# Optimization experiments

Hardware: AMD Instinct MI355X
Metric: run time of the kernel (lower is better)

Reference implementation:

```python
import jax, jax.numpy as jnp
import numpy as np

B, T, DIM = 2, 1024, 4096
H, Hk, D = 32, 8, 128
NREP = H // Hk
SCALE = 1.0 / np.sqrt(D)
LAMBDA_INIT = 0.8 - 0.6 * np.exp(-0.3 * 0)  # layer_idx=0 -> 0.2
EPS = 1e-6


def setup_inputs() -> dict:
    key = jax.random.key(0)
    ks = jax.random.split(key, 12)
    x = jax.random.normal(ks[0], (B, T, DIM), dtype=jnp.float32)
    cos = jax.random.uniform(ks[1], (T, D // 2), dtype=jnp.float32)
    sin = jax.random.uniform(ks[2], (T, D // 2), dtype=jnp.float32)
    wq = jax.random.normal(ks[3], (DIM, 2 * H * D), dtype=jnp.float32) * 0.02
    wk = jax.random.normal(ks[4], (DIM, 2 * Hk * D), dtype=jnp.float32) * 0.02
    wv = jax.random.normal(ks[5], (DIM, Hk * D), dtype=jnp.float32) * 0.02
    wo = jax.random.normal(ks[6], (H * D, DIM), dtype=jnp.float32) * 0.02
    lambda_q1 = jax.random.normal(ks[7], (H, D), dtype=jnp.float32) * 0.1
    lambda_k1 = jax.random.normal(ks[8], (H, D), dtype=jnp.float32) * 0.1
    lambda_q2 = jax.random.normal(ks[9], (H, D), dtype=jnp.float32) * 0.1
    lambda_k2 = jax.random.normal(ks[10], (H, D), dtype=jnp.float32) * 0.1
    subln_w = jnp.ones((D,), dtype=jnp.float32)
    return {"x": x, "cos": cos, "sin": sin, "wq": wq, "wk": wk, "wv": wv,
            "wo": wo, "lambda_q1": lambda_q1, "lambda_k1": lambda_k1,
            "lambda_q2": lambda_q2, "lambda_k2": lambda_k2, "subln_w": subln_w}


def _rope(xh, cos, sin):
    # xh: [B, h, T, D]; cos/sin: [T, D/2]
    x1, x2 = xh[..., : D // 2], xh[..., D // 2:]
    c = cos[None, None, :, :]
    s = sin[None, None, :, :]
    return jnp.concatenate([x1 * c - x2 * s, x2 * c + x1 * s], axis=-1)


def _causal_attn(q, k, v):
    # q,k,v: [B, H, T, D]
    s = jnp.einsum("bhqd,bhkd->bhqk", q, k) * SCALE
    causal = jnp.tril(jnp.ones((T, T), dtype=bool))
    s = jnp.where(causal[None, None], s, jnp.finfo(s.dtype).min)
    p = jax.nn.softmax(s, axis=-1)
    return jnp.einsum("bhqk,bhkd->bhqd", p, v)


def reference(x, cos, sin, wq, wk, wv, wo, lambda_q1, lambda_k1, lambda_q2, lambda_k2, subln_w):
    q_full = (x @ wq).reshape(B, T, 2 * H, D).transpose(0, 2, 1, 3)   # [B,2H,T,D]
    k_full = (x @ wk).reshape(B, T, 2 * Hk, D).transpose(0, 2, 1, 3)  # [B,2Hk,T,D]
    v = (x @ wv).reshape(B, T, Hk, D).transpose(0, 2, 1, 3)           # [B,Hk,T,D]

    q1, q2 = q_full[:, :H], q_full[:, H:]
    k1, k2 = k_full[:, :Hk], k_full[:, Hk:]

    q1 = _rope(q1, cos, sin)
    q2 = _rope(q2, cos, sin)
    k1 = _rope(k1, cos, sin)
    k2 = _rope(k2, cos, sin)

    def expand_kv(kv):  # [B,Hk,T,D] -> [B,H,T,D] (GQA repeat)
        return jnp.repeat(kv, NREP, axis=1)

    k1e, k2e, ve = expand_kv(k1), expand_kv(k2), expand_kv(v)

    a1 = _causal_attn(q1, k1e, ve)
    a2 = _causal_attn(q2, k2e, ve)

    lam = (jnp.exp(jnp.sum(lambda_q1 * lambda_k1, axis=-1))
           - jnp.exp(jnp.sum(lambda_q2 * lambda_k2, axis=-1))
           + LAMBDA_INIT)  # [H]
    diff = a1 - lam[None, :, None, None] * a2  # [B,H,T,D]

    # per-head-dim RMSNorm (subln)
    rms = jax.lax.rsqrt(jnp.mean(diff * diff, axis=-1, keepdims=True) + EPS)
    diff = diff * rms * subln_w

    out = diff.transpose(0, 2, 1, 3).reshape(B, T, H * D)
    return out @ wo
```

## Files before the change

### kernel.cpp

```cpp
#include <hip/hip_runtime.h>
#include <hip/hip_bf16.h>
#include <stdint.h>

typedef unsigned short u16;
typedef unsigned int u32;
typedef short bf16x8 __attribute__((ext_vector_type(8)));
typedef float f32x4 __attribute__((ext_vector_type(4)));

#define SCALE_F 0.088388347648318447f
#define LAMBDA_INIT_F 0.2f

__device__ __forceinline__ u16 f2bf(float f) {
  union { float f; u32 u; } v; v.f = f;
  u32 r = v.u + 0x7fffu + ((v.u >> 16) & 1u);
  return (u16)(r >> 16);
}
__device__ __forceinline__ float bf2f(u16 u) {
  union { u32 u; float f; } v; v.u = ((u32)u) << 16;
  return v.f;
}

typedef __attribute__((address_space(1))) void gvoid_t;
typedef __attribute__((address_space(3))) void lvoid_t;
__device__ __forceinline__ void gload16(const void* g, void* l) {
  __builtin_amdgcn_global_load_lds((gvoid_t*)g, (lvoid_t*)l, 16, 0, 0);
}

__global__ void cast_f32_bf16(const float4* __restrict__ in, uint2* __restrict__ out, int n4) {
  int i = blockIdx.x * 256 + threadIdx.x;
  if (i >= n4) return;
  float4 v = in[i];
  uint2 o;
  o.x = (u32)f2bf(v.x) | ((u32)f2bf(v.y) << 16);
  o.y = (u32)f2bf(v.z) | ((u32)f2bf(v.w) << 16);
  out[i] = o;
}

__global__ void trans_cast(const float* __restrict__ in, u16* __restrict__ out, int K, int N) {
  __shared__ float tile[32][33];
  int kt = blockIdx.y * 32, nt = blockIdx.x * 32;
  int x = threadIdx.x, y = threadIdx.y;
  #pragma unroll
  for (int j = 0; j < 32; j += 8)
    tile[y + j][x] = in[(size_t)(kt + y + j) * N + nt + x];
  __syncthreads();
  #pragma unroll
  for (int j = 0; j < 32; j += 8)
    out[(size_t)(nt + y + j) * K + kt + x] = f2bf(tile[x][y + j]);
}

#define STA(buf, t) { \
  gload16(Ab + (size_t)(t) * 64, (buf) + dsloc); \
  gload16(Ab + (size_t)32 * K + (size_t)(t) * 64, (buf) + 2048 + dsloc); \
  gload16(Ab + (size_t)64 * K + (size_t)(t) * 64, (buf) + 4096 + dsloc); \
  gload16(Ab + (size_t)96 * K + (size_t)(t) * 64, (buf) + 6144 + dsloc); }
#define STB(buf, t) { \
  gload16(Bb + (size_t)(t) * 64, (buf) + dsloc); \
  gload16(Bb + (size_t)32 * K + (size_t)(t) * 64, (buf) + 2048 + dsloc); \
  gload16(Bb + (size_t)64 * K + (size_t)(t) * 64, (buf) + 4096 + dsloc); \
  gload16(Bb + (size_t)96 * K + (size_t)(t) * 64, (buf) + 6144 + dsloc); }
#define MFMA16 { \
  acc[0][0] = __builtin_amdgcn_mfma_f32_16x16x32_bf16(a0, b0, acc[0][0], 0, 0, 0); \
  acc[0][1] = __builtin_amdgcn_mfma_f32_16x16x32_bf16(a0, b1, acc[0][1], 0, 0, 0); \
  acc[0][2] = __builtin_amdgcn_mfma_f32_16x16x32_bf16(a0, b2, acc[0][2], 0, 0, 0); \
  acc[0][3] = __builtin_amdgcn_mfma_f32_16x16x32_bf16(a0, b3, acc[0][3], 0, 0, 0); \
  acc[1][0] = __builtin_amdgcn_mfma_f32_16x16x32_bf16(a1, b0, acc[1][0], 0, 0, 0); \
  acc[1][1] = __builtin_amdgcn_mfma_f32_16x16x32_bf16(a1, b1, acc[1][1], 0, 0, 0); \
  acc[1][2] = __builtin_amdgcn_mfma_f32_16x16x32_bf16(a1, b2, acc[1][2], 0, 0, 0); \
  acc[1][3] = __builtin_amdgcn_mfma_f32_16x16x32_bf16(a1, b3, acc[1][3], 0, 0, 0); \
  acc[2][0] = __builtin_amdgcn_mfma_f32_16x16x32_bf16(a2, b0, acc[2][0], 0, 0, 0); \
  acc[2][1] = __builtin_amdgcn_mfma_f32_16x16x32_bf16(a2, b1, acc[2][1], 0, 0, 0); \
  acc[2][2] = __builtin_amdgcn_mfma_f32_16x16x32_bf16(a2, b2, acc[2][2], 0, 0, 0); \
  acc[2][3] = __builtin_amdgcn_mfma_f32_16x16x32_bf16(a2, b3, acc[2][3], 0, 0, 0); \
  acc[3][0] = __builtin_amdgcn_mfma_f32_16x16x32_bf16(a3, b0, acc[3][0], 0, 0, 0); \
  acc[3][1] = __builtin_amdgcn_mfma_f32_16x16x32_bf16(a3, b1, acc[3][1], 0, 0, 0); \
  acc[3][2] = __builtin_amdgcn_mfma_f32_16x16x32_bf16(a3, b2, acc[3][2], 0, 0, 0); \
  acc[3][3] = __builtin_amdgcn_mfma_f32_16x16x32_bf16(a3, b3, acc[3][3], 0, 0, 0); }

template <bool OUT_BF16>
__global__ __launch_bounds__(256, 2) void gemm8p(const u16* __restrict__ A,
                                                 const u16* __restrict__ Bt,
                                                 void* __restrict__ Cv,
                                                 int M, int N, int K, int TN) {
  extern __shared__ u16 lds[];
  const int tid = threadIdx.x;
  const int lane = tid & 63;
  const int wid = tid >> 6;
  const int wm = wid >> 1, wn = wid & 1;
  const int ln = lane & 15, gr = lane >> 4;
  const int NT = K >> 6;

  const int bid = blockIdx.x;
  const int bn = (bid % TN) * 128;
  const int bm = (bid / TN) * 128;

  const int srow = tid >> 3;
  const int sch = (tid & 7) ^ (srow & 7);
  const u16* Ab = A + (size_t)(bm + srow) * K + sch * 8;
  const u16* Bb = Bt + (size_t)(bn + srow) * K + sch * 8;
  const int dsloc = tid * 8;

  const int aro = (wm * 64 + ln) * 64;
  const int bro = (wn * 64 + ln) * 64;
  const int c0 = (gr ^ (ln & 7)) * 8;
  const int c1 = ((4 + gr) ^ (ln & 7)) * 8;

  f32x4 acc[4][4] = {};
  bf16x8 a0, a1, a2, a3, b0, b1, b2, b3;

  STA(lds, 0);
  STB(lds + 16384, 0);
  STB(lds + 24576, 1);
  asm volatile("s_waitcnt vmcnt(4)" ::: "memory");
  __builtin_amdgcn_s_barrier();

  int tm3 = 0;
  for (int t = 0; t < NT; ++t) {
    const u16* Ac = lds + (t & 1) * 8192;
    u16* An = lds + ((t + 1) & 1) * 8192;
    const u16* Bc = lds + 16384 + tm3 * 8192;
    int tn3 = tm3 + 2; if (tn3 >= 3) tn3 -= 3;
    u16* Bn = lds + 16384 + tn3 * 8192;

    a0 = *(const bf16x8*)&Ac[aro + c0];
    a1 = *(const bf16x8*)&Ac[aro + 1024 + c0];
    a2 = *(const bf16x8*)&Ac[aro + 2048 + c0];
    a3 = *(const bf16x8*)&Ac[aro + 3072 + c0];
    b0 = *(const bf16x8*)&Bc[bro + c0];
    b1 = *(const bf16x8*)&Bc[bro + 1024 + c0];
    b2 = *(const bf16x8*)&Bc[bro + 2048 + c0];
    b3 = *(const bf16x8*)&Bc[bro + 3072 + c0];
    if (t + 1 < NT) STA(An, t + 1);
    __builtin_amdgcn_s_barrier();
    __builtin_amdgcn_s_setprio(1);
    MFMA16;
    __builtin_amdgcn_s_setprio(0);
    __builtin_amdgcn_s_barrier();

    a0 = *(const bf16x8*)&Ac[aro + c1];
    a1 = *(const bf16x8*)&Ac[aro + 1024 + c1];
    a2 = *(const bf16x8*)&Ac[aro + 2048 + c1];
    a3 = *(const bf16x8*)&Ac[aro + 3072 + c1];
    b0 = *(const bf16x8*)&Bc[bro + c1];
    b1 = *(const bf16x8*)&Bc[bro + 1024 + c1];
    b2 = *(const bf16x8*)&Bc[bro + 2048 + c1];
    b3 = *(const bf16x8*)&Bc[bro + 3072 + c1];
    if (t + 2 < NT) {
      STB(Bn, t + 2);
      asm volatile("s_waitcnt vmcnt(4)" ::: "memory");
    } else {
      asm volatile("s_waitcnt vmcnt(0)" ::: "memory");
    }
    __builtin_amdgcn_s_barrier();
    __builtin_amdgcn_s_setprio(1);
    MFMA16;
    __builtin_amdgcn_s_setprio(0);
    __builtin_amdgcn_s_barrier();

    tm3 = (tm3 + 1 == 3) ? 0 : tm3 + 1;
  }

  #pragma unroll
  for (int mf = 0; mf < 4; ++mf) {
    #pragma unroll
    for (int j = 0; j < 4; ++j) {
      int r = bm + wm * 64 + mf * 16 + gr * 4 + j;
      #pragma unroll
      for (int nf = 0; nf < 4; ++nf) {
        int c = bn + wn * 64 + nf * 16 + ln;
        if (OUT_BF16) ((u16*)Cv)[(size_t)r * N + c] = f2bf(acc[mf][nf][j]);
        else          ((float*)Cv)[(size_t)r * N + c] = acc[mf][nf][j];
      }
    }
  }
}

__global__ void rope_kernel(const u16* __restrict__ in, u16* __restrict__ out,
                            const float* __restrict__ cosp, const float* __restrict__ sinp,
                            int NHh, int col_off) {
  int idx = blockIdx.x * 256 + threadIdx.x;
  int d = idx & 63;
  int t = (idx >> 6) & 1023;
  int h = (idx >> 16) % NHh;
  int b = (idx >> 16) / NHh;
  size_t src = (size_t)(b * 1024 + t) * 11264 + col_off + h * 128;
  float x1 = bf2f(in[src + d]);
  float x2 = bf2f(in[src + 64 + d]);
  float c = cosp[t * 64 + d], s = sinp[t * 64 + d];
  size_t dst = ((size_t)(b * NHh + h) * 1024 + t) * 128;
  out[dst + d] = f2bf(x1 * c - x2 * s);
  out[dst + 64 + d] = f2bf(x2 * c + x1 * s);
}

__global__ void vtrans_kernel(const u16* __restrict__ qkv, u16* __restrict__ vt) {
  __shared__ u16 tile[32][34];
  int bh = blockIdx.z;
  int t0 = blockIdx.x * 32, d0 = blockIdx.y * 32;
  int b = bh >> 3, hk = bh & 7;
  int x = threadIdx.x, y = threadIdx.y;
  #pragma unroll
  for (int j = 0; j < 32; j += 8)
    tile[y + j][x] = qkv[(size_t)(b * 1024 + t0 + y + j) * 11264 + 10240 + hk * 128 + d0 + x];
  __syncthreads();
  #pragma unroll
  for (int j = 0; j < 32; j += 8)
    vt[((size_t)bh * 128 + d0 + y + j) * 1024 + t0 + x] = tile[x][y + j];
}

__global__ void lam_kernel(const float* __restrict__ lq1, const float* __restrict__ lk1,
                           const float* __restrict__ lq2, const float* __restrict__ lk2,
                           float* __restrict__ lam) {
  int h = blockIdx.x, l = threadIdx.x;
  float p1 = lq1[h * 128 + l] * lk1[h * 128 + l] + lq1[h * 128 + 64 + l] * lk1[h * 128 + 64 + l];
  float p2 = lq2[h * 128 + l] * lk2[h * 128 + l] + lq2[h * 128 + 64 + l] * lk2[h * 128 + 64 + l];
  #pragma unroll
  for (int m = 32; m >= 1; m >>= 1) { p1 += __shfl_xor(p1, m); p2 += __shfl_xor(p2, m); }
  if (l == 0) lam[h] = expf(p1) - expf(p2) + LAMBDA_INIT_F;
}

__global__ __launch_bounds__(256) void attn_kernel(const u16* __restrict__ qr,
                                                   const u16* __restrict__ kr,
                                                   const u16* __restrict__ vt,
                                                   const float* __restrict__ lam,
                                                   const float* __restrict__ slw,
                                                   u16* __restrict__ attno) {
  __shared__ u16 k1s[32 * 136];
  __shared__ u16 k2s[32 * 136];
  __shared__ u16 vs[128 * 40];
  __shared__ u16 ps[4][2][640];
  const int qt = 15 - (int)blockIdx.x;
  const int h = blockIdx.y, b = blockIdx.z;
  const int tid = threadIdx.x, lane = tid & 63, w = tid >> 6;
  const int ln = lane & 15, gr = lane >> 4;
  const int hk = h >> 2;
  const int qrow0 = qt * 64 + w * 16;
  u16* psw1 = ps[w][0];
  u16* psw2 = ps[w][1];
  const float SL2E = 0.12751744006165926f;
  const float ML2E = 11.541560327111707f;

  bf16x8 q1f[4], q2f[4];
  {
    const u16* q1p = qr + ((size_t)(b * 64 + h) * 1024 + qrow0 + ln) * 128 + gr * 8;
    const u16* q2p = qr + ((size_t)(b * 64 + 32 + h) * 1024 + qrow0 + ln) * 128 + gr * 8;
    #pragma unroll
    for (int ds = 0; ds < 4; ++ds) {
      q1f[ds] = *(const bf16x8*)(q1p + ds * 32);
      q2f[ds] = *(const bf16x8*)(q2p + ds * 32);
    }
  }
  f32x4 acc1[8] = {}, acc2[8] = {};
  float l1[4] = {0.f, 0.f, 0.f, 0.f}, l2[4] = {0.f, 0.f, 0.f, 0.f};

  const u16* k1g = kr + (size_t)(b * 16 + hk) * 1024 * 128;
  const u16* k2g = kr + (size_t)(b * 16 + 8 + hk) * 1024 * 128;
  const u16* vg = vt + (size_t)(b * 8 + hk) * 128 * 1024;
  const int nkt = 2 * qt + 2;

  for (int kt = 0; kt < nkt; ++kt) {
    #pragma unroll
    for (int c = 0; c < 2; ++c) {
      int row = c * 16 + (tid >> 4);
      int ch = tid & 15;
      *(bf16x8*)&k1s[row * 136 + ch * 8] = *(const bf16x8*)&k1g[(size_t)(kt * 32 + row) * 128 + ch * 8];
      *(bf16x8*)&k2s[row * 136 + ch * 8] = *(const bf16x8*)&k2g[(size_t)(kt * 32 + row) * 128 + ch * 8];
      int dr = c * 64 + (tid >> 2);
      int ch2 = tid & 3;
      *(bf16x8*)&vs[dr * 40 + ch2 * 8] = *(const bf16x8*)&vg[(size_t)dr * 1024 + kt * 32 + ch2 * 8];
    }
    __syncthreads();

    f32x4 s1[2], s2[2];
    #pragma unroll
    for (int ct = 0; ct < 2; ++ct) {
      s1[ct] = (f32x4){0.f, 0.f, 0.f, 0.f};
      s2[ct] = (f32x4){0.f, 0.f, 0.f, 0.f};
      #pragma unroll
      for (int ds = 0; ds < 4; ++ds) {
        bf16x8 kf1 = *(const bf16x8*)&k1s[(ct * 16 + ln) * 136 + ds * 32 + gr * 8];
        s1[ct] = __builtin_amdgcn_mfma_f32_16x16x32_bf16(q1f[ds], kf1, s1[ct], 0, 0, 0);
        bf16x8 kf2 = *(const bf16x8*)&k2s[(ct * 16 + ln) * 136 + ds * 32 + gr * 8];
        s2[ct] = __builtin_amdgcn_mfma_f32_16x16x32_bf16(q2f[ds], kf2, s2[ct], 0, 0, 0);
      }
    }
    #pragma unroll
    for (int j = 0; j < 4; ++j) {
      int row = qrow0 + gr * 4 + j;
      bool msk0 = (kt * 32 + ln) > row;
      bool msk1 = (kt * 32 + 16 + ln) > row;
      float t10 = msk0 ? -1e30f : fmaf(s1[0][j], SL2E, -ML2E);
      float t11 = msk1 ? -1e30f : fmaf(s1[1][j], SL2E, -ML2E);
      float t20 = msk0 ? -1e30f : fmaf(s2[0][j], SL2E, -ML2E);
      float t21 = msk1 ? -1e30f : fmaf(s2[1][j], SL2E, -ML2E);
      u16 b10 = f2bf(exp2f(t10)), b11 = f2bf(exp2f(t11));
      u16 b20 = f2bf(exp2f(t20)), b21 = f2bf(exp2f(t21));
      int ro = (gr * 4 + j) * 40;
      psw1[ro + ln] = b10; psw1[ro + 16 + ln] = b11;
      psw2[ro + ln] = b20; psw2[ro + 16 + ln] = b21;
      l1[j] += bf2f(b10) + bf2f(b11);
      l2[j] += bf2f(b20) + bf2f(b21);
    }
    bf16x8 pf1 = *(const bf16x8*)&psw1[ln * 40 + gr * 8];
    bf16x8 pf2 = *(const bf16x8*)&psw2[ln * 40 + gr * 8];
    #pragma unroll
    for (int dt = 0; dt < 8; ++dt) {
      bf16x8 vf = *(const bf16x8*)&vs[(dt * 16 + ln) * 40 + gr * 8];
      acc1[dt] = __builtin_amdgcn_mfma_f32_16x16x32_bf16(pf1, vf, acc1[dt], 0, 0, 0);
      acc2[dt] = __builtin_amdgcn_mfma_f32_16x16x32_bf16(pf2, vf, acc2[dt], 0, 0, 0);
    }
    __syncthreads();
  }

  float inv1[4], inv2[4];
  #pragma unroll
  for (int j = 0; j < 4; ++j) {
    float a = l1[j], c = l2[j];
    a += __shfl_xor(a, 1); a += __shfl_xor(a, 2); a += __shfl_xor(a, 4); a += __shfl_xor(a, 8);
    c += __shfl_xor(c, 1); c += __shfl_xor(c, 2); c += __shfl_xor(c, 4); c += __shfl_xor(c, 8);
    inv1[j] = 1.f / a;
    inv2[j] = 1.f / c;
  }

  float lamv = lam[h];
  float ssq[4] = {0.f, 0.f, 0.f, 0.f};
  #pragma unroll
  for (int dt = 0; dt < 8; ++dt)
    #pragma unroll
    for (int j = 0; j < 4; ++j) {
      float d = acc1[dt][j] * inv1[j] - lamv * (acc2[dt][j] * inv2[j]);
      acc1[dt][j] = d;
      ssq[j] += d * d;
    }
  #pragma unroll
  for (int j = 0; j < 4; ++j) {
    float s = ssq[j];
    s += __shfl_xor(s, 1);
    s += __shfl_xor(s, 2);
    s += __shfl_xor(s, 4);
    s += __shfl_xor(s, 8);
    ssq[j] = rsqrtf(s * (1.0f / 128.0f) + 1e-6f);
  }
  #pragma unroll
  for (int dt = 0; dt < 8; ++dt) {
    float wgt = slw[dt * 16 + ln];
    #pragma unroll
    for (int j = 0; j < 4; ++j) {
      int row = qrow0 + gr * 4 + j;
      attno[(size_t)(b * 1024 + row) * 4096 + h * 128 + dt * 16 + ln] = f2bf(acc1[dt][j] * ssq[j] * wgt);
    }
  }
}

extern "C" void kernel_launch(void* const* d_in, const int* in_sizes, int n_in,
                              void* d_out, int out_size, void* d_ws, size_t ws_size,
                              hipStream_t stream) {
  (void)in_sizes; (void)n_in; (void)out_size; (void)ws_size;
  const float* x    = (const float*)d_in[0];
  const float* cosp = (const float*)d_in[1];
  const float* sinp = (const float*)d_in[2];
  const float* wq   = (const float*)d_in[3];
  const float* wk   = (const float*)d_in[4];
  const float* wv   = (const float*)d_in[5];
  const float* wo   = (const float*)d_in[6];
  const float* lq1  = (const float*)d_in[7];
  const float* lk1  = (const float*)d_in[8];
  const float* lq2  = (const float*)d_in[9];
  const float* lk2  = (const float*)d_in[10];
  const float* slw  = (const float*)d_in[11];
  float* out = (float*)d_out;
  char* ws = (char*)d_ws;

  u16* xb    = (u16*)(ws);
  u16* wqkvt = (u16*)(ws + 16777216);
  u16* qr    = (u16*)(ws + 16777216);
  u16* kr    = (u16*)(ws + 50331648);
  u16* vtp   = (u16*)(ws + 58720256);
  u16* attno = (u16*)(ws + 62914560);
  u16* qkv   = (u16*)(ws + 109051904);
  u16* wot   = (u16*)(ws + 109051904);
  float* lam = (float*)(ws + 155189248);

  cast_f32_bf16<<<8192, 256, 0, stream>>>((const float4*)x, (uint2*)xb, 2097152);
  trans_cast<<<dim3(256, 128), dim3(32, 8), 0, stream>>>(wq, wqkvt, 4096, 8192);
  trans_cast<<<dim3(64, 128),  dim3(32, 8), 0, stream>>>(wk, wqkvt + (size_t)8192 * 4096, 4096, 2048);
  trans_cast<<<dim3(32, 128),  dim3(32, 8), 0, stream>>>(wv, wqkvt + (size_t)10240 * 4096, 4096, 1024);
  gemm8p<true><<<1408, 256, 81920, stream>>>(xb, wqkvt, (void*)qkv, 2048, 11264, 4096, 88);
  rope_kernel<<<32768, 256, 0, stream>>>(qkv, qr, cosp, sinp, 64, 0);
  rope_kernel<<<8192, 256, 0, stream>>>(qkv, kr, cosp, sinp, 16, 8192);
  vtrans_kernel<<<dim3(32, 4, 16), dim3(32, 8), 0, stream>>>(qkv, vtp);
  trans_cast<<<dim3(128, 128), dim3(32, 8), 0, stream>>>(wo, wot, 4096, 4096);
  lam_kernel<<<32, 64, 0, stream>>>(lq1, lk1, lq2, lk2, lam);
  attn_kernel<<<dim3(16, 32, 2), 256, 0, stream>>>(qr, kr, vtp, lam, slw, attno);
  gemm8p<false><<<512, 256, 81920, stream>>>(attno, wot, (void*)out, 2048, 4096, 4096, 32);
}
```

Measured before the change: 478.7 us.

## Add 128x256 triple-buffered GEMM kernel for the QKV projection

Adds a new bf16 GEMM kernel (gemmW) with a 128x256 output tile, K-step of 32, three-stage LDS ring buffering with split A/B prefetch, and swizzled LDS addressing, and uses it for the QKV projection instead of gemm8p. The larger N tile raises per-block reuse of the A operand and halves the block count, aiming to cut global/LDS traffic and barrier overhead per FLOP. It costs 128 fp32 accumulators per thread (register pressure, two blocks per CU) and a smaller grid (704 blocks), which may hurt occupancy or wave-quantization balance.

```diff
diff --git a/kernel.cpp b/kernel.cpp
--- a/kernel.cpp
+++ b/kernel.cpp
@@ -47,6 +47,122 @@
   #pragma unroll
   for (int j = 0; j < 32; j += 8)
     out[(size_t)(nt + y + j) * K + kt + x] = f2bf(tile[x][y + j]);
+}
+
+#define SQA(buf, t) { \
+  gload16(Aq + (size_t)(t) * 32, (buf) + qdst); \
+  gload16(Aq + (size_t)64 * K + (size_t)(t) * 32, (buf) + 2048 + qdst); }
+#define SQB(buf, t) { \
+  gload16(Bq + (size_t)(t) * 32, (buf) + qdst); \
+  gload16(Bq + (size_t)64 * K + (size_t)(t) * 32, (buf) + 2048 + qdst); \
+  gload16(Bq + (size_t)128 * K + (size_t)(t) * 32, (buf) + 4096 + qdst); \
+  gload16(Bq + (size_t)192 * K + (size_t)(t) * 32, (buf) + 6144 + qdst); }
+#define QMFMA16(O) { \
+  acc[O+0][0] = __builtin_amdgcn_mfma_f32_16x16x32_bf16(a0, b0, acc[O+0][0], 0, 0, 0); \
+  acc[O+0][1] = __builtin_amdgcn_mfma_f32_16x16x32_bf16(a0, b1, acc[O+0][1], 0, 0, 0); \
+  acc[O+0][2] = __builtin_amdgcn_mfma_f32_16x16x32_bf16(a0, b2, acc[O+0][2], 0, 0, 0); \
+  acc[O+0][3] = __builtin_amdgcn_mfma_f32_16x16x32_bf16(a0, b3, acc[O+0][3], 0, 0, 0); \
+  acc[O+1][0] = __builtin_amdgcn_mfma_f32_16x16x32_bf16(a1, b0, acc[O+1][0], 0, 0, 0); \
+  acc[O+1][1] = __builtin_amdgcn_mfma_f32_16x16x32_bf16(a1, b1, acc[O+1][1], 0, 0, 0); \
+  acc[O+1][2] = __builtin_amdgcn_mfma_f32_16x16x32_bf16(a1, b2, acc[O+1][2], 0, 0, 0); \
+  acc[O+1][3] = __builtin_amdgcn_mfma_f32_16x16x32_bf16(a1, b3, acc[O+1][3], 0, 0, 0); \
+  acc[O+2][0] = __builtin_amdgcn_mfma_f32_16x16x32_bf16(a2, b0, acc[O+2][0], 0, 0, 0); \
+  acc[O+2][1] = __builtin_amdgcn_mfma_f32_16x16x32_bf16(a2, b1, acc[O+2][1], 0, 0, 0); \
+  acc[O+2][2] = __builtin_amdgcn_mfma_f32_16x16x32_bf16(a2, b2, acc[O+2][2], 0, 0, 0); \
+  acc[O+2][3] = __builtin_amdgcn_mfma_f32_16x16x32_bf16(a2, b3, acc[O+2][3], 0, 0, 0); \
+  acc[O+3][0] = __builtin_amdgcn_mfma_f32_16x16x32_bf16(a3, b0, acc[O+3][0], 0, 0, 0); \
+  acc[O+3][1] = __builtin_amdgcn_mfma_f32_16x16x32_bf16(a3, b1, acc[O+3][1], 0, 0, 0); \
+  acc[O+3][2] = __builtin_amdgcn_mfma_f32_16x16x32_bf16(a3, b2, acc[O+3][2], 0, 0, 0); \
+  acc[O+3][3] = __builtin_amdgcn_mfma_f32_16x16x32_bf16(a3, b3, acc[O+3][3], 0, 0, 0); }
+
+__global__ __launch_bounds__(256, 2) void gemmW(const u16* __restrict__ A,
+                                                const u16* __restrict__ Bt,
+                                                u16* __restrict__ C,
+                                                int M, int N, int K, int TN) {
+  extern __shared__ u16 lds[];
+  const int tid = threadIdx.x;
+  const int lane = tid & 63;
+  const int wn = tid >> 6;
+  const int ln = lane & 15, gr = lane >> 4;
+  const int NT = K >> 5;
+
+  const int bid = blockIdx.x;
+  const int bn = (bid % TN) * 256;
+  const int bm = (bid / TN) * 128;
+
+  const int sch = (tid & 3) ^ ((tid >> 3) & 3);
+  const u16* Aq = A + (size_t)(bm + (tid >> 2)) * K + sch * 8;
+  const u16* Bq = Bt + (size_t)(bn + (tid >> 2)) * K + sch * 8;
+  const int qdst = tid * 8;
+
+  const int cfo = (gr ^ ((ln >> 1) & 3)) * 8;
+  const int ab = ln * 32 + cfo;
+  const int bb = wn * 2048 + ln * 32 + cfo;
+
+  f32x4 acc[8][4] = {};
+  bf16x8 a0, a1, a2, a3, b0, b1, b2, b3;
+
+  SQA(lds, 0);
+  SQB(lds + 12288, 0);
+  SQA(lds + 4096, 1);
+  SQB(lds + 20480, 1);
+  asm volatile("s_waitcnt vmcnt(6)" ::: "memory");
+  __builtin_amdgcn_s_barrier();
+
+  int tm3 = 0;
+  for (int t = 0; t < NT; ++t) {
+    const u16* Ac = lds + tm3 * 4096;
+    const u16* Bc = lds + 12288 + tm3 * 8192;
+    int tn3 = tm3 + 2; if (tn3 >= 3) tn3 -= 3;
+    u16* An = lds + tn3 * 4096;
+    u16* Bn = lds + 12288 + tn3 * 8192;
+
+    a0 = *(const bf16x8*)&Ac[ab];
+    a1 = *(const bf16x8*)&Ac[ab + 512];
+    a2 = *(const bf16x8*)&Ac[ab + 1024];
+    a3 = *(const bf16x8*)&Ac[ab + 1536];
+    b0 = *(const bf16x8*)&Bc[bb];
+    b1 = *(const bf16x8*)&Bc[bb + 512];
+    b2 = *(const bf16x8*)&Bc[bb + 1024];
+    b3 = *(const bf16x8*)&Bc[bb + 1536];
+    if (t + 2 < NT) SQA(An, t + 2);
+    __builtin_amdgcn_s_barrier();
+    __builtin_amdgcn_s_setprio(1);
+    QMFMA16(0);
+    __builtin_amdgcn_s_setprio(0);
+    __builtin_amdgcn_s_barrier();
+
+    a0 = *(const bf16x8*)&Ac[ab + 2048];
+    a1 = *(const bf16x8*)&Ac[ab + 2560];
+    a2 = *(const bf16x8*)&Ac[ab + 3072];
+    a3 = *(const bf16x8*)&Ac[ab + 3584];
+    if (t + 2 < NT) {
+      SQB(Bn, t + 2);
+      asm volatile("s_waitcnt vmcnt(6)" ::: "memory");
+    } else {
+      asm volatile("s_waitcnt vmcnt(0)" ::: "memory");
+    }
+    __builtin_amdgcn_s_barrier();
+    __builtin_amdgcn_s_setprio(1);
+    QMFMA16(4);
+    __builtin_amdgcn_s_setprio(0);
+    __builtin_amdgcn_s_barrier();
+
+    tm3 = (tm3 + 1 == 3) ? 0 : tm3 + 1;
+  }
+
+  #pragma unroll
+  for (int mf = 0; mf < 8; ++mf) {
+    #pragma unroll
+    for (int j = 0; j < 4; ++j) {
+      int r = bm + mf * 16 + gr * 4 + j;
+      #pragma unroll
+      for (int nf = 0; nf < 4; ++nf) {
+        int c = bn + wn * 64 + nf * 16 + ln;
+        C[(size_t)r * N + c] = f2bf(acc[mf][nf][j]);
+      }
+    }
+  }
 }
 
 #define STA(buf, t) { \
@@ -384,7 +500,7 @@
   trans_cast<<<dim3(256, 128), dim3(32, 8), 0, stream>>>(wq, wqkvt, 4096, 8192);
   trans_cast<<<dim3(64, 128),  dim3(32, 8), 0, stream>>>(wk, wqkvt + (size_t)8192 * 4096, 4096, 2048);
   trans_cast<<<dim3(32, 128),  dim3(32, 8), 0, stream>>>(wv, wqkvt + (size_t)10240 * 4096, 4096, 1024);
-  gemm8p<true><<<1408, 256, 81920, stream>>>(xb, wqkvt, (void*)qkv, 2048, 11264, 4096, 88);
+  gemmW<<<704, 256, 73728, stream>>>(xb, wqkvt, qkv, 2048, 11264, 4096, 44);
   rope_kernel<<<32768, 256, 0, stream>>>(qkv, qr, cosp, sinp, 64, 0);
   rope_kernel<<<8192, 256, 0, stream>>>(qkv, kr, cosp, sinp, 16, 8192);
   vtrans_kernel<<<dim3(32, 4, 16), dim3(32, 8), 0, stream>>>(qkv, vtp);
```

After: 493.2 us. 3.0% more time.

## Add 128x256 GEMM streaming B from registers for the QKV projection

Applied to the files above, without the earlier changes.

Adds a new GEMM kernel for the fused QKV projection. Each wave streams its 64 B columns straight from global memory into registers. Only A tiles (128x32) go through a triple-buffered LDS ring with a swizzled layout, which reduces LDS use to 24 KB and allows two blocks per CU. The larger 128x256 tile halves the grid and raises MFMA reuse per A fragment. The cost is direct global B loads with per-lane stride-K access and higher register pressure from 32 accumulators, and the unswizzled direct register loads may be less coalesced.

```diff
diff --git a/kernel.cpp b/kernel.cpp
--- a/kernel.cpp
+++ b/kernel.cpp
@@ -47,6 +47,132 @@
   #pragma unroll
   for (int j = 0; j < 32; j += 8)
     out[(size_t)(nt + y + j) * K + kt + x] = f2bf(tile[x][y + j]);
+}
+
+#define SQA(buf, t) { \
+  gload16(Aq + (size_t)(t) * 32, (buf) + qdst); \
+  gload16(Aq + (size_t)64 * K + (size_t)(t) * 32, (buf) + 2048 + qdst); }
+#define QMFMA16(O, B0, B1, B2, B3) { \
+  acc[O+0][0] = __builtin_amdgcn_mfma_f32_16x16x32_bf16(a0, B0, acc[O+0][0], 0, 0, 0); \
+  acc[O+0][1] = __builtin_amdgcn_mfma_f32_16x16x32_bf16(a0, B1, acc[O+0][1], 0, 0, 0); \
+  acc[O+0][2] = __builtin_amdgcn_mfma_f32_16x16x32_bf16(a0, B2, acc[O+0][2], 0, 0, 0); \
+  acc[O+0][3] = __builtin_amdgcn_mfma_f32_16x16x32_bf16(a0, B3, acc[O+0][3], 0, 0, 0); \
+  acc[O+1][0] = __builtin_amdgcn_mfma_f32_16x16x32_bf16(a1, B0, acc[O+1][0], 0, 0, 0); \
+  acc[O+1][1] = __builtin_amdgcn_mfma_f32_16x16x32_bf16(a1, B1, acc[O+1][1], 0, 0, 0); \
+  acc[O+1][2] = __builtin_amdgcn_mfma_f32_16x16x32_bf16(a1, B2, acc[O+1][2], 0, 0, 0); \
+  acc[O+1][3] = __builtin_amdgcn_mfma_f32_16x16x32_bf16(a1, B3, acc[O+1][3], 0, 0, 0); \
+  acc[O+2][0] = __builtin_amdgcn_mfma_f32_16x16x32_bf16(a2, B0, acc[O+2][0], 0, 0, 0); \
+  acc[O+2][1] = __builtin_amdgcn_mfma_f32_16x16x32_bf16(a2, B1, acc[O+2][1], 0, 0, 0); \
+  acc[O+2][2] = __builtin_amdgcn_mfma_f32_16x16x32_bf16(a2, B2, acc[O+2][2], 0, 0, 0); \
+  acc[O+2][3] = __builtin_amdgcn_mfma_f32_16x16x32_bf16(a2, B3, acc[O+2][3], 0, 0, 0); \
+  acc[O+3][0] = __builtin_amdgcn_mfma_f32_16x16x32_bf16(a3, B0, acc[O+3][0], 0, 0, 0); \
+  acc[O+3][1] = __builtin_amdgcn_mfma_f32_16x16x32_bf16(a3, B1, acc[O+3][1], 0, 0, 0); \
+  acc[O+3][2] = __builtin_amdgcn_mfma_f32_16x16x32_bf16(a3, B2, acc[O+3][2], 0, 0, 0); \
+  acc[O+3][3] = __builtin_amdgcn_mfma_f32_16x16x32_bf16(a3, B3, acc[O+3][3], 0, 0, 0); }
+#define RDA(buf, off) { \
+  a0 = *(const bf16x8*)&(buf)[ab + (off)]; \
+  a1 = *(const bf16x8*)&(buf)[ab + (off) + 512]; \
+  a2 = *(const bf16x8*)&(buf)[ab + (off) + 1024]; \
+  a3 = *(const bf16x8*)&(buf)[ab + (off) + 1536]; }
+
+__global__ __launch_bounds__(256, 2) void gemmW(const u16* __restrict__ A,
+                                                const u16* __restrict__ Bt,
+                                                u16* __restrict__ C,
+                                                int M, int N, int K, int TN) {
+  extern __shared__ u16 lds[];
+  const int tid = threadIdx.x;
+  const int lane = tid & 63;
+  const int wn = tid >> 6;
+  const int ln = lane & 15, gr = lane >> 4;
+  const int NT = K >> 5;
+
+  const int bid = blockIdx.x;
+  const int bn = (bid % TN) * 256;
+  const int bm = (bid / TN) * 128;
+
+  const int sch = (tid & 3) ^ ((tid >> 3) & 3);
+  const u16* Aq = A + (size_t)(bm + (tid >> 2)) * K + sch * 8;
+  const int qdst = tid * 8;
+
+  const u16* Bp0 = Bt + (size_t)(bn + wn * 64 + ln) * K + gr * 8;
+  const u16* Bp1 = Bp0 + (size_t)16 * K;
+  const u16* Bp2 = Bp0 + (size_t)32 * K;
+  const u16* Bp3 = Bp0 + (size_t)48 * K;
+
+  const int cfo = (gr ^ ((ln >> 1) & 3)) * 8;
+  const int ab = ln * 32 + cfo;
+
+  f32x4 acc[8][4] = {};
+  bf16x8 a0, a1, a2, a3;
+  bf16x8 x0, x1, x2, x3, y0, y1, y2, y3;
+
+  SQA(lds, 0);
+  x0 = *(const bf16x8*)(Bp0);
+  x1 = *(const bf16x8*)(Bp1);
+  x2 = *(const bf16x8*)(Bp2);
+  x3 = *(const bf16x8*)(Bp3);
+  SQA(lds + 4096, 1);
+
+  int tm3 = 0;
+  for (int t = 0; t < NT; t += 2) {
+    int n1 = tm3 + 1; if (n1 >= 3) n1 -= 3;
+    int n2 = tm3 + 2; if (n2 >= 3) n2 -= 3;
+    const u16* Ac0 = lds + tm3 * 4096;
+    const u16* Ac1 = lds + n1 * 4096;
+    u16* Aw2 = lds + n2 * 4096;
+    u16* Aw3 = lds + tm3 * 4096;
+
+    y0 = *(const bf16x8*)(Bp0 + (size_t)(t + 1) * 32);
+    y1 = *(const bf16x8*)(Bp1 + (size_t)(t + 1) * 32);
+    y2 = *(const bf16x8*)(Bp2 + (size_t)(t + 1) * 32);
+    y3 = *(const bf16x8*)(Bp3 + (size_t)(t + 1) * 32);
+    asm volatile("s_waitcnt vmcnt(6)" ::: "memory");
+    __builtin_amdgcn_s_barrier();
+    RDA(Ac0, 0);
+    __builtin_amdgcn_s_setprio(1);
+    QMFMA16(0, x0, x1, x2, x3);
+    __builtin_amdgcn_s_setprio(0);
+    if (t + 2 < NT) SQA(Aw2, t + 2);
+    RDA(Ac0, 2048);
+    __builtin_amdgcn_s_setprio(1);
+    QMFMA16(4, x0, x1, x2, x3);
+    __builtin_amdgcn_s_setprio(0);
+
+    if (t + 2 < NT) {
+      x0 = *(const bf16x8*)(Bp0 + (size_t)(t + 2) * 32);
+      x1 = *(const bf16x8*)(Bp1 + (size_t)(t + 2) * 32);
+      x2 = *(const bf16x8*)(Bp2 + (size_t)(t + 2) * 32);
+      x3 = *(const bf16x8*)(Bp3 + (size_t)(t + 2) * 32);
+      asm volatile("s_waitcnt vmcnt(6)" ::: "memory");
+    } else {
+      asm volatile("s_waitcnt vmcnt(0)" ::: "memory");
+    }
+    __builtin_amdgcn_s_barrier();
+    RDA(Ac1, 0);
+    __builtin_amdgcn_s_setprio(1);
+    QMFMA16(0, y0, y1, y2, y3);
+    __builtin_amdgcn_s_setprio(0);
+    if (t + 3 < NT) SQA(Aw3, t + 3);
+    RDA(Ac1, 2048);
+    __builtin_amdgcn_s_setprio(1);
+    QMFMA16(4, y0, y1, y2, y3);
+    __builtin_amdgcn_s_setprio(0);
+
+    tm3 = n2;
+  }
+
+  #pragma unroll
+  for (int mf = 0; mf < 8; ++mf) {
+    #pragma unroll
+    for (int j = 0; j < 4; ++j) {
+      int r = bm + mf * 16 + gr * 4 + j;
+      #pragma unroll
+      for (int nf = 0; nf < 4; ++nf) {
+        int c = bn + wn * 64 + nf * 16 + ln;
+        C[(size_t)r * N + c] = f2bf(acc[mf][nf][j]);
+      }
+    }
+  }
 }
 
 #define STA(buf, t) { \
@@ -384,7 +510,7 @@
   trans_cast<<<dim3(256, 128), dim3(32, 8), 0, stream>>>(wq, wqkvt, 4096, 8192);
   trans_cast<<<dim3(64, 128),  dim3(32, 8), 0, stream>>>(wk, wqkvt + (size_t)8192 * 4096, 4096, 2048);
   trans_cast<<<dim3(32, 128),  dim3(32, 8), 0, stream>>>(wv, wqkvt + (size_t)10240 * 4096, 4096, 1024);
-  gemm8p<true><<<1408, 256, 81920, stream>>>(xb, wqkvt, (void*)qkv, 2048, 11264, 4096, 88);
+  gemmW<<<704, 256, 24576, stream>>>(xb, wqkvt, qkv, 2048, 11264, 4096, 44);
   rope_kernel<<<32768, 256, 0, stream>>>(qkv, qr, cosp, sinp, 64, 0);
   rope_kernel<<<8192, 256, 0, stream>>>(qkv, kr, cosp, sinp, 16, 8192);
   vtrans_kernel<<<dim3(32, 4, 16), dim3(32, 8), 0, stream>>>(qkv, vtp);
```

New measurement: 531.9 us. 1.11x slower.
